# Performance work log

Measured on AMD Instinct MI355X. Metric: run time of the kernel, lower is better.

## Reference

```python
import jax, jax.numpy as jnp
import numpy as np

N_ITERS = 50

def sinkhorn_knopp(W, n_iters=N_ITERS):
    # Project W onto the Birkhoff polytope via alternating row/col normalization.
    W = jnp.abs(W) + 1e-8
    def body(i, W):
        W = W / jnp.sum(W, axis=-1, keepdims=True)  # row-normalize
        W = W / jnp.sum(W, axis=-2, keepdims=True)  # col-normalize
        return W
    return jax.lax.fori_loop(0, n_iters, body, W)

def setup_inputs() -> dict:
    key = jax.random.key(0)
    k1, k2, k3 = jax.random.split(key, 3)
    residual = jax.random.normal(k1, (2, 4096, 4096), dtype=jnp.float32)
    sublayer_out = jax.random.normal(k2, (2, 4096, 4096), dtype=jnp.float32)
    # Mimic init: eye(2)*2 + 0.01*randn
    W_raw = jnp.eye(2, dtype=jnp.float32) * 2.0 + 0.01 * jax.random.normal(k3, (2, 2), dtype=jnp.float32)
    return {"residual": residual, "sublayer_out": sublayer_out, "W_raw": W_raw}

def reference(residual, sublayer_out, W_raw):
    W = sinkhorn_knopp(W_raw, N_ITERS)
    # stream_0 + stream_1 = (W00+W10)*residual + (W01+W11)*sublayer_out
    a = W[0, 0] + W[1, 0]
    b = W[0, 1] + W[1, 1]
    return a * residual + b * sublayer_out
```

## Files before the change

kernel.cpp:

```cpp
#include <hip/hip_runtime.h>

#define SK_ITERS 50

__global__ __launch_bounds__(256) void sinkhorn_mix_kernel(
    const float* __restrict__ residual,
    const float* __restrict__ sublayer,
    const float* __restrict__ W_raw,
    float* __restrict__ out,
    long long n)
{
    __shared__ float s_ab[2];

    if (threadIdx.x == 0) {
        float w00 = fabsf(W_raw[0]) + 1e-8f;
        float w01 = fabsf(W_raw[1]) + 1e-8f;
        float w10 = fabsf(W_raw[2]) + 1e-8f;
        float w11 = fabsf(W_raw[3]) + 1e-8f;
        #pragma unroll 1
        for (int i = 0; i < SK_ITERS; ++i) {
            float r0 = w00 + w01;
            float r1 = w10 + w11;
            w00 = w00 / r0; w01 = w01 / r0;
            w10 = w10 / r1; w11 = w11 / r1;
            float c0 = w00 + w10;
            float c1 = w01 + w11;
            w00 = w00 / c0; w10 = w10 / c0;
            w01 = w01 / c1; w11 = w11 / c1;
        }
        s_ab[0] = w00 + w10;
        s_ab[1] = w01 + w11;
    }
    __syncthreads();

    const float a = s_ab[0];
    const float b = s_ab[1];

    const long long n4 = n >> 2;
    const float4* __restrict__ r4 = reinterpret_cast<const float4*>(residual);
    const float4* __restrict__ s4 = reinterpret_cast<const float4*>(sublayer);
    float4* __restrict__ o4 = reinterpret_cast<float4*>(out);

    const long long tid    = (long long)blockIdx.x * blockDim.x + threadIdx.x;
    const long long stride = (long long)gridDim.x * blockDim.x;

    for (long long i = tid; i < n4; i += stride) {
        float4 rv = r4[i];
        float4 sv = s4[i];
        float4 ov;
        ov.x = a * rv.x + b * sv.x;
        ov.y = a * rv.y + b * sv.y;
        ov.z = a * rv.z + b * sv.z;
        ov.w = a * rv.w + b * sv.w;
        o4[i] = ov;
    }

    for (long long i = (n4 << 2) + tid; i < n; i += stride) {
        out[i] = a * residual[i] + b * sublayer[i];
    }
}

extern "C" void kernel_launch(void* const* d_in, const int* in_sizes, int n_in,
                              void* d_out, int out_size, void* d_ws, size_t ws_size,
                              hipStream_t stream) {
    const float* residual = (const float*)d_in[0];
    const float* sublayer = (const float*)d_in[1];
    const float* W_raw    = (const float*)d_in[2];
    float* out            = (float*)d_out;

    const long long n = (long long)out_size;

    const int block = 256;
    const int grid  = 2048;

    sinkhorn_mix_kernel<<<grid, block, 0, stream>>>(residual, sublayer, W_raw, out, n);
}
```

Measured before the change: 320.3 us.

## Issue loads before Sinkhorn prologue, one-shot grid with 8 vectors per thread

Replaces the grid-stride loop with a grid sized to cover the data exactly, where each thread handles 8 float4 elements. All loads are issued before thread 0 computes the Sinkhorn coefficients, so memory latency overlaps the serial 50-iteration prologue. Divisions become reciprocal-multiplies, and output stores use nontemporal hints. The trade-off is more blocks, each redundantly running the serial Sinkhorn loop, and higher register pressure from 16 live float4 values per thread.

```diff
diff --git a/kernel.cpp b/kernel.cpp
--- a/kernel.cpp
+++ b/kernel.cpp
@@ -1,61 +1,91 @@
 #include <hip/hip_runtime.h>
 
+
+typedef float f4 __attribute__((ext_vector_type(4)));
+
 #define SK_ITERS 50
+constexpr int BLOCK = 256;
+constexpr int VPT   = 8;
+constexpr int CPB   = BLOCK * VPT;
 
-__global__ __launch_bounds__(256) void sinkhorn_mix_kernel(
-    const float* __restrict__ residual,
-    const float* __restrict__ sublayer,
+__device__ __forceinline__ void sinkhorn_ab(const float* __restrict__ W,
+                                            float& a, float& b) {
+    float w00 = fabsf(W[0]) + 1e-8f;
+    float w01 = fabsf(W[1]) + 1e-8f;
+    float w10 = fabsf(W[2]) + 1e-8f;
+    float w11 = fabsf(W[3]) + 1e-8f;
+    #pragma unroll 1
+    for (int i = 0; i < SK_ITERS; ++i) {
+        float t0 = 1.0f / (w00 + w01);
+        float t1 = 1.0f / (w10 + w11);
+        w00 *= t0; w01 *= t0; w10 *= t1; w11 *= t1;
+        float u0 = 1.0f / (w00 + w10);
+        float u1 = 1.0f / (w01 + w11);
+        w00 *= u0; w10 *= u0; w01 *= u1; w11 *= u1;
+    }
+    a = w00 + w10;
+    b = w01 + w11;
+}
+
+__global__ __launch_bounds__(BLOCK) void sinkhorn_mix_kernel(
+    const f4* __restrict__ r4, const f4* __restrict__ s4, f4* __restrict__ o4,
     const float* __restrict__ W_raw,
-    float* __restrict__ out,
-    long long n)
+    const float* __restrict__ rs, const float* __restrict__ ss,
+    float* __restrict__ os,
+    long long n4, long long n)
 {
     __shared__ float s_ab[2];
 
+    const long long blockStart = (long long)blockIdx.x * CPB;
+    const long long tbase      = blockStart + threadIdx.x;
+    const bool full = (blockStart + CPB) <= n4;
+
+    f4 rv[VPT], sv[VPT];
+
+    if (full) {
+        #pragma unroll
+        for (int k = 0; k < VPT; ++k) rv[k] = r4[tbase + (long long)k * BLOCK];
+        #pragma unroll
+        for (int k = 0; k < VPT; ++k) sv[k] = s4[tbase + (long long)k * BLOCK];
+    }
+
     if (threadIdx.x == 0) {
-        float w00 = fabsf(W_raw[0]) + 1e-8f;
-        float w01 = fabsf(W_raw[1]) + 1e-8f;
-        float w10 = fabsf(W_raw[2]) + 1e-8f;
-        float w11 = fabsf(W_raw[3]) + 1e-8f;
-        #pragma unroll 1
-        for (int i = 0; i < SK_ITERS; ++i) {
-            float r0 = w00 + w01;
-            float r1 = w10 + w11;
-            w00 = w00 / r0; w01 = w01 / r0;
-            w10 = w10 / r1; w11 = w11 / r1;
-            float c0 = w00 + w10;
-            float c1 = w01 + w11;
-            w00 = w00 / c0; w10 = w10 / c0;
-            w01 = w01 / c1; w11 = w11 / c1;
-        }
-        s_ab[0] = w00 + w10;
-        s_ab[1] = w01 + w11;
+        float a, b;
+        sinkhorn_ab(W_raw, a, b);
+        s_ab[0] = a; s_ab[1] = b;
     }
     __syncthreads();
+    const float a = s_ab[0], b = s_ab[1];
 
-    const float a = s_ab[0];
-    const float b = s_ab[1];
-
-    const long long n4 = n >> 2;
-    const float4* __restrict__ r4 = reinterpret_cast<const float4*>(residual);
-    const float4* __restrict__ s4 = reinterpret_cast<const float4*>(sublayer);
-    float4* __restrict__ o4 = reinterpret_cast<float4*>(out);
-
-    const long long tid    = (long long)blockIdx.x * blockDim.x + threadIdx.x;
-    const long long stride = (long long)gridDim.x * blockDim.x;
-
-    for (long long i = tid; i < n4; i += stride) {
-        float4 rv = r4[i];
-        float4 sv = s4[i];
-        float4 ov;
-        ov.x = a * rv.x + b * sv.x;
-        ov.y = a * rv.y + b * sv.y;
-        ov.z = a * rv.z + b * sv.z;
-        ov.w = a * rv.w + b * sv.w;
-        o4[i] = ov;
-    }
-
-    for (long long i = (n4 << 2) + tid; i < n; i += stride) {
-        out[i] = a * residual[i] + b * sublayer[i];
+    if (full) {
+        #pragma unroll
+        for (int k = 0; k < VPT; ++k) {
+            f4 ov;
+            ov.x = a * rv[k].x + b * sv[k].x;
+            ov.y = a * rv[k].y + b * sv[k].y;
+            ov.z = a * rv[k].z + b * sv[k].z;
+            ov.w = a * rv[k].w + b * sv[k].w;
+            __builtin_nontemporal_store(ov, &o4[tbase + (long long)k * BLOCK]);
+        }
+    } else {
+        #pragma unroll 1
+        for (int k = 0; k < VPT; ++k) {
+            long long i = tbase + (long long)k * BLOCK;
+            if (i < n4) {
+                f4 rvk = r4[i], svk = s4[i];
+                f4 ov;
+                ov.x = a * rvk.x + b * svk.x;
+                ov.y = a * rvk.y + b * svk.y;
+                ov.z = a * rvk.z + b * svk.z;
+                ov.w = a * rvk.w + b * svk.w;
+                o4[i] = ov;
+            }
+        }
+        if (blockIdx.x == (int)gridDim.x - 1) {
+            for (long long e = 4 * n4 + threadIdx.x; e < n; e += BLOCK) {
+                os[e] = a * rs[e] + b * ss[e];
+            }
+        }
     }
 }
 
@@ -67,10 +97,13 @@
     const float* W_raw    = (const float*)d_in[2];
     float* out            = (float*)d_out;
 
-    const long long n = (long long)out_size;
+    const long long n  = (long long)out_size;
+    const long long n4 = n >> 2;
 
-    const int block = 256;
-    const int grid  = 2048;
+    long long grid = (n4 + CPB - 1) / CPB;
+    if (grid < 1) grid = 1;
 
-    sinkhorn_mix_kernel<<<grid, block, 0, stream>>>(residual, sublayer, W_raw, out, n);
+    sinkhorn_mix_kernel<<<(int)grid, BLOCK, 0, stream>>>(
+        (const f4*)residual, (const f4*)sublayer, (f4*)out, W_raw,
+        residual, sublayer, out, n4, n);
 }
```

Measured after the change: 323.8 us. No clear change (+1.1%).
